# Kernel optimization log

Measured on AMD Instinct MI355X. Metric: run time of the kernel, lower is better.

Reference implementation:

```python
import jax, jax.numpy as jnp
import numpy as np

D_MODEL = 256; D_FFN = 1024; N_LEVELS = 4; N_HEADS = 8; N_POINTS = 4; N_VT = 8
D_HEAD = D_MODEL // N_HEADS
SHAPES = [(64, 64), (32, 32), (16, 16), (8, 8)]
L_SP = sum(h * w for h, w in SHAPES)  # 5440
BATCH = 4
EPS = 1e-5


def _ln(x, g, b):
    m = jnp.mean(x, -1, keepdims=True)
    xc = x - m
    v = jnp.mean(xc * xc, -1, keepdims=True)
    return g * xc * jax.lax.rsqrt(v + EPS) + b


def _bilinear(v_flat, x, y, H, W):
    # v_flat: (N, H*W, M, Dh); x, y: (N, Q, M) pixel coords (align_corners=False, zero padding)
    x0 = jnp.floor(x); y0 = jnp.floor(y)
    wx = x - x0; wy = y - y0
    out = 0.0
    for cx, cy, w in ((x0, y0, (1 - wx) * (1 - wy)), (x0 + 1, y0, wx * (1 - wy)),
                      (x0, y0 + 1, (1 - wx) * wy), (x0 + 1, y0 + 1, wx * wy)):
        valid = (cx >= 0) & (cx < W) & (cy >= 0) & (cy < H)
        xi = jnp.clip(cx, 0, W - 1).astype(jnp.int32)
        yi = jnp.clip(cy, 0, H - 1).astype(jnp.int32)
        idx = (yi * W + xi)[..., None]  # (N, Q, M, 1)
        g = jnp.take_along_axis(v_flat, idx, axis=1)  # (N, Q, M, Dh)
        out = out + (w * valid)[..., None] * g
    return out


def _msdeform_attn(query, ref, value_in, shapes_np, pad_mask, Wv, bv, Wo, bo, Wa, ba, Wp, bp):
    N, Lq, D = query.shape
    M, Lv, P, Dh = N_HEADS, N_LEVELS, N_POINTS, D_HEAD
    value = value_in @ Wv.T + bv
    value = jnp.where(pad_mask[..., None], 0.0, value)
    value = value.reshape(N, Lq, M, Dh)
    off = (query @ Wo.T + bo).reshape(N, Lq, M, Lv, P, 2)
    attn = jax.nn.softmax((query @ Wa.T + ba).reshape(N, Lq, M, Lv * P), axis=-1)
    attn = attn.reshape(N, Lq, M, Lv, P)
    # offset normalizer is (W, H) per level
    normalizer = jnp.asarray([[w, h] for h, w in shapes_np], jnp.float32)
    loc = ref[:, :, None, :, None, :] + off / normalizer[None, None, None, :, None, :]
    out = 0.0
    start = 0
    for l, (H, W) in enumerate(shapes_np):
        v_l = value[:, start:start + H * W]  # (N, H*W, M, Dh)
        x = (loc[:, :, :, l, :, 0] * W - 0.5).transpose(0, 1, 3, 2).reshape(N, Lq * P, M)
        y = (loc[:, :, :, l, :, 1] * H - 0.5).transpose(0, 1, 3, 2).reshape(N, Lq * P, M)
        samp = _bilinear(v_l, x, y, H, W).reshape(N, Lq, P, M, Dh)
        out = out + jnp.einsum('nqpmd,nqmp->nqmd', samp, attn[:, :, :, l, :])
        start += H * W
    return out.reshape(N, Lq, D) @ Wp.T + bp


def setup_inputs() -> dict:
    key = jax.random.key(0)
    ks = jax.random.split(key, 16)
    N, D = BATCH, D_MODEL
    Lq = L_SP + N_VT
    s = D ** -0.5
    rn = lambda k, sh, sc=1.0: jax.random.normal(k, sh, dtype=jnp.float32) * sc
    starts = np.cumsum([0] + [h * w for h, w in SHAPES[:-1]])
    return {
        'src': rn(ks[0], (N, L_SP, D)),
        'pos': rn(ks[1], (N, L_SP, D), 0.1),
        'reference_points': jax.random.uniform(ks[2], (N, Lq, N_LEVELS, 2), dtype=jnp.float32),
        'spatial_shapes': jnp.asarray(SHAPES, jnp.int32),
        'level_start_index': jnp.asarray(starts, jnp.int32),
        'padding_mask': jnp.zeros((N, Lq), bool),
        'all_vt': rn(ks[3], (N, 75 * N_VT, D)),
        'sel_vt': rn(ks[4], (N, N_VT, D)),
        'W_value': rn(ks[5], (D, D), s), 'b_value': jnp.zeros((D,), jnp.float32),
        'W_off': rn(ks[6], (N_HEADS * N_LEVELS * N_POINTS * 2, D), s),
        'b_off': rn(ks[7], (N_HEADS * N_LEVELS * N_POINTS * 2,), 0.1),
        'W_attn': rn(ks[8], (N_HEADS * N_LEVELS * N_POINTS, D), s),
        'b_attn': jnp.zeros((N_HEADS * N_LEVELS * N_POINTS,), jnp.float32),
        'W_out': rn(ks[9], (D, D), s), 'b_out': jnp.zeros((D,), jnp.float32),
        'g1': jnp.ones((D,), jnp.float32), 'beta1': jnp.zeros((D,), jnp.float32),
        'W1': rn(ks[10], (D_FFN, D), s), 'bf1': jnp.zeros((D_FFN,), jnp.float32),
        'W2': rn(ks[11], (D, D_FFN), D_FFN ** -0.5), 'bf2': jnp.zeros((D,), jnp.float32),
        'g2': jnp.ones((D,), jnp.float32), 'beta2': jnp.zeros((D,), jnp.float32),
    }


def reference(src, pos, reference_points, spatial_shapes, level_start_index, padding_mask,
              all_vt, sel_vt, W_value, b_value, W_off, b_off, W_attn, b_attn, W_out, b_out,
              g1, beta1, W1, bf1, W2, bf2, g2, beta2):
    shapes_np = [tuple(int(v) for v in row) for row in np.asarray(spatial_shapes)]
    q = jnp.concatenate([src + pos, sel_vt], axis=1)      # (N, Lq, D)
    v_in = jnp.concatenate([src, sel_vt], axis=1)
    src2 = _msdeform_attn(q, reference_points, v_in, shapes_np, padding_mask,
                          W_value, b_value, W_off, b_off, W_attn, b_attn, W_out, b_out)
    x = _ln(v_in + src2, g1, beta1)
    h = jax.nn.relu(x @ W1.T + bf1) @ W2.T + bf2
    x = _ln(x + h, g2, beta2)
    return (x[:, :L_SP, :], all_vt, x[:, L_SP:, :])
```

## Files before the change

kernel.cpp:

```cpp
#include <hip/hip_runtime.h>
#include <math.h>

#define NB   4
#define LQ   5448
#define LSP  5440
#define NR   21792
#define DM   256

typedef unsigned short u16;
typedef __attribute__((ext_vector_type(8))) short short8;
typedef __attribute__((ext_vector_type(4))) float f32x4;
typedef __attribute__((ext_vector_type(4))) unsigned int uint4v;

__device__ __forceinline__ u16 f2bf(float f) {
  unsigned int u = __float_as_uint(f);
  u = (u + 0x7fff + ((u >> 16) & 1)) >> 16;
  return (u16)u;
}
__device__ __forceinline__ float bf2f(u16 u) {
  return __uint_as_float(((unsigned int)u) << 16);
}

__device__ __forceinline__ void gld_lds16(const u16* g, u16* l) {
  __builtin_amdgcn_global_load_lds(
      (const __attribute__((address_space(1))) void*)g,
      (__attribute__((address_space(3))) void*)l, 16, 0, 0);
}

#define OFF_R0 0ull
#define OFF_R1 44630016ull
#define OFF_R2 55787520ull
#define OFF_R3 66945024ull
#define OFF_WB 78102528ull
#define OFF_BI 79609856ull

#define WOF_V  0
#define WOF_OA 65536
#define WOF_P  163840
#define WOF_1  229376
#define WOF_2  491520
#define NWELEM 753664

#define OUT0 5570560ull
#define OUT1 614400ull

__global__ __launch_bounds__(256) void convw_k(
    const float* __restrict__ Wv, const float* __restrict__ Wo,
    const float* __restrict__ Wa, const float* __restrict__ Wp,
    const float* __restrict__ W1, const float* __restrict__ W2,
    const float* __restrict__ bo, const float* __restrict__ ba,
    u16* __restrict__ out, float* __restrict__ boa)
{
  const int gid = blockIdx.x * 256 + threadIdx.x;
  if (gid < 384) boa[gid] = (gid < 256) ? bo[gid] : ba[gid - 256];
  if (gid >= NWELEM) return;
  float v;
  if (gid < WOF_OA) {
    v = Wv[gid];
  } else if (gid < WOF_P) {
    const int o = gid - WOF_OA;
    v = (o < 65536) ? Wo[o] : Wa[o - 65536];
  } else if (gid < WOF_1) {
    v = Wp[gid - WOF_P];
  } else if (gid < WOF_2) {
    v = W1[gid - WOF_1];
  } else {
    v = W2[gid - WOF_2];
  }
  out[gid] = f2bf(v);
}

__global__ __launch_bounds__(256) void qv_build_k(
    const float* __restrict__ src, const float* __restrict__ pos,
    const float* __restrict__ sel,
    u16* __restrict__ qb, u16* __restrict__ vb)
{
  const int row = blockIdx.x * 4 + (threadIdx.x >> 6);
  const int t = threadIdx.x & 63;
  const int n = row / LQ;
  const int i = row - n * LQ;
  float4 v, p = make_float4(0.f, 0.f, 0.f, 0.f);
  if (i < LSP) {
    const size_t o = ((size_t)(n * LSP + i)) * DM + t * 4;
    v = *(const float4*)(src + o);
    p = *(const float4*)(pos + o);
  } else {
    v = *(const float4*)(sel + ((size_t)(n * 8 + (i - LSP))) * DM + t * 4);
  }
  ushort4 vq, vv;
  vv.x = f2bf(v.x); vv.y = f2bf(v.y); vv.z = f2bf(v.z); vv.w = f2bf(v.w);
  vq.x = f2bf(v.x + p.x); vq.y = f2bf(v.y + p.y);
  vq.z = f2bf(v.z + p.z); vq.w = f2bf(v.w + p.w);
  *(ushort4*)(vb + (size_t)row * DM + t * 4) = vv;
  *(ushort4*)(qb + (size_t)row * DM + t * 4) = vq;
}

__global__ __launch_bounds__(256) void gemm_oa_k(
    const u16* __restrict__ A, int lda,
    const u16* __restrict__ B, int ldb,
    const float* __restrict__ bias,
    float* __restrict__ C, int ldc, int M, int K)
{
  __shared__ u16 As[128 * 32];
  __shared__ u16 Bs[128 * 32];
  const int tid = threadIdx.x;
  const int m0 = blockIdx.y * 128;
  const int n0 = blockIdx.x * 128;
  const int w = tid >> 6, lane = tid & 63;
  const int wy = w >> 1, wx = w & 1;
  const int l15 = lane & 15, quad = lane >> 4;
  const int lrow = lane >> 2;
  const int ga8 = ((lane & 3) ^ ((lane >> 3) & 3)) * 8;
  const int swz = (quad ^ ((l15 >> 1) & 3)) * 8;

  f32x4 acc[4][4] = {};

  for (int k0 = 0; k0 < K; k0 += 32) {
    for (int s = w; s < 8; s += 4) {
      int gm = m0 + s * 16 + lrow;
      if (gm >= M) gm = M - 1;
      gld_lds16(A + (size_t)gm * lda + k0 + ga8, &As[s * 512]);
    }
    for (int s = w; s < 8; s += 4) {
      gld_lds16(B + (size_t)(n0 + s * 16 + lrow) * ldb + k0 + ga8, &Bs[s * 512]);
    }
    __syncthreads();
    short8 af[4], bfr[4];
#pragma unroll
    for (int r = 0; r < 4; ++r)
      af[r] = *(const short8*)&As[(wy * 64 + r * 16 + l15) * 32 + swz];
#pragma unroll
    for (int c = 0; c < 4; ++c)
      bfr[c] = *(const short8*)&Bs[(wx * 64 + c * 16 + l15) * 32 + swz];
#pragma unroll
    for (int r = 0; r < 4; ++r)
#pragma unroll
      for (int c = 0; c < 4; ++c)
        acc[r][c] = __builtin_amdgcn_mfma_f32_16x16x32_bf16(af[r], bfr[c], acc[r][c], 0, 0, 0);
    __syncthreads();
  }

#pragma unroll
  for (int c = 0; c < 4; ++c) {
    const int cc = n0 + wx * 64 + c * 16 + l15;
    const float bb = bias[cc];
#pragma unroll
    for (int r = 0; r < 4; ++r) {
      const int rbase = m0 + wy * 64 + r * 16 + quad * 4;
#pragma unroll
      for (int j = 0; j < 4; ++j) {
        const int gr = rbase + j;
        if (gr < M) C[(size_t)gr * ldc + cc] = acc[r][c][j] + bb;
      }
    }
  }
}

template <int EPI>
__global__ __launch_bounds__(256) void gemmT_k(
    const u16* __restrict__ A, int lda,
    const u16* __restrict__ B, int ldb,
    const float* __restrict__ bias, int K,
    u16* __restrict__ outb, int ldob,
    const float* __restrict__ src, const float* __restrict__ sel,
    const u16* __restrict__ xbf,
    const float* __restrict__ gvec, const float* __restrict__ bvec,
    float* __restrict__ outf)
{
  __shared__ u16 As[64 * 32];
  __shared__ u16 Bs[256 * 32];
  const int tid = threadIdx.x;
  const int m0 = blockIdx.y * 64;
  const int n0 = blockIdx.x * 256;
  const int w = tid >> 6, lane = tid & 63;
  const int l15 = lane & 15, quad = lane >> 4;
  const int lrow = lane >> 2;
  const int ga8 = ((lane & 3) ^ ((lane >> 3) & 3)) * 8;
  const int swz = (quad ^ ((l15 >> 1) & 3)) * 8;

  f32x4 acc[4][4] = {};

  for (int k0 = 0; k0 < K; k0 += 32) {
    {
      int gm = m0 + w * 16 + lrow;
      if (gm >= NR) gm = NR - 1;
      gld_lds16(A + (size_t)gm * lda + k0 + ga8, &As[w * 512]);
    }
#pragma unroll
    for (int t = 0; t < 4; ++t) {
      const int s = w * 4 + t;
      gld_lds16(B + (size_t)(n0 + s * 16 + lrow) * ldb + k0 + ga8, &Bs[s * 512]);
    }
    __syncthreads();
    short8 af[4], bfr[4];
#pragma unroll
    for (int r = 0; r < 4; ++r)
      af[r] = *(const short8*)&As[(r * 16 + l15) * 32 + swz];
#pragma unroll
    for (int c = 0; c < 4; ++c)
      bfr[c] = *(const short8*)&Bs[(w * 64 + c * 16 + l15) * 32 + swz];
#pragma unroll
    for (int r = 0; r < 4; ++r)
#pragma unroll
      for (int c = 0; c < 4; ++c)
        acc[r][c] = __builtin_amdgcn_mfma_f32_16x16x32_bf16(af[r], bfr[c], acc[r][c], 0, 0, 0);
    __syncthreads();
  }

  int col[4];
  float bb[4];
#pragma unroll
  for (int c = 0; c < 4; ++c) {
    col[c] = n0 + w * 64 + c * 16 + l15;
    bb[c] = bias[col[c]];
  }

  if (EPI <= 1) {
#pragma unroll
    for (int c = 0; c < 4; ++c) {
#pragma unroll
      for (int r = 0; r < 4; ++r) {
#pragma unroll
        for (int j = 0; j < 4; ++j) {
          const int row = m0 + r * 16 + quad * 4 + j;
          if (row < NR) {
            float v = acc[r][c][j] + bb[c];
            if (EPI == 1) v = fmaxf(v, 0.f);
            outb[(size_t)row * ldob + col[c]] = f2bf(v);
          }
        }
      }
    }
    return;
  }

  float sv[4][4], sq[4][4];
#pragma unroll
  for (int r = 0; r < 4; ++r) {
#pragma unroll
    for (int j = 0; j < 4; ++j) {
      const int row = m0 + r * 16 + quad * 4 + j;
      const int rc = (row < NR) ? row : NR - 1;
      if (EPI == 2) {
        const int n = rc / LQ;
        const int i = rc - n * LQ;
        const float* resb = (i < LSP)
            ? src + ((size_t)(n * LSP + i)) * DM
            : sel + ((size_t)(n * 8 + (i - LSP))) * DM;
#pragma unroll
        for (int c = 0; c < 4; ++c) acc[r][c][j] += bb[c] + resb[col[c]];
      } else {
#pragma unroll
        for (int c = 0; c < 4; ++c)
          acc[r][c][j] += bb[c] + bf2f(xbf[(size_t)rc * DM + col[c]]);
      }
      float s = 0.f, q = 0.f;
#pragma unroll
      for (int c = 0; c < 4; ++c) {
        const float v = acc[r][c][j];
        s += v; q += v * v;
      }
      sv[r][j] = s; sq[r][j] = q;
    }
  }
#pragma unroll
  for (int off = 1; off < 16; off <<= 1) {
#pragma unroll
    for (int r = 0; r < 4; ++r)
#pragma unroll
      for (int j = 0; j < 4; ++j) {
        sv[r][j] += __shfl_xor(sv[r][j], off, 64);
        sq[r][j] += __shfl_xor(sq[r][j], off, 64);
      }
  }
  float* red = (float*)As;
  if (l15 == 0) {
#pragma unroll
    for (int r = 0; r < 4; ++r)
#pragma unroll
      for (int j = 0; j < 4; ++j) {
        const int rl = r * 16 + quad * 4 + j;
        red[(rl * 4 + w) * 2 + 0] = sv[r][j];
        red[(rl * 4 + w) * 2 + 1] = sq[r][j];
      }
  }
  __syncthreads();

  float gg[4], b2[4];
#pragma unroll
  for (int c = 0; c < 4; ++c) { gg[c] = gvec[col[c]]; b2[c] = bvec[col[c]]; }

#pragma unroll
  for (int r = 0; r < 4; ++r) {
#pragma unroll
    for (int j = 0; j < 4; ++j) {
      const int row = m0 + r * 16 + quad * 4 + j;
      if (row >= NR) continue;
      const int rl = r * 16 + quad * 4 + j;
      float ms = 0.f, mq = 0.f;
#pragma unroll
      for (int ww = 0; ww < 4; ++ww) {
        ms += red[(rl * 4 + ww) * 2 + 0];
        mq += red[(rl * 4 + ww) * 2 + 1];
      }
      const float mean = ms * (1.f / 256.f);
      const float var = mq * (1.f / 256.f) - mean * mean;
      const float rin = rsqrtf(var + 1e-5f);
      if (EPI == 2) {
#pragma unroll
        for (int c = 0; c < 4; ++c) {
          const float v = gg[c] * (acc[r][c][j] - mean) * rin + b2[c];
          outb[(size_t)row * DM + col[c]] = f2bf(v);
        }
      } else {
        const int n = row / LQ;
        const int i = row - n * LQ;
        float* dst = (i < LSP)
            ? outf + (size_t)(n * LSP + i) * DM
            : outf + OUT0 + OUT1 + (size_t)(n * 8 + (i - LSP)) * DM;
#pragma unroll
        for (int c = 0; c < 4; ++c)
          dst[col[c]] = gg[c] * (acc[r][c][j] - mean) * rin + b2[c];
      }
    }
  }
}

__device__ __forceinline__ void acc8(float* a, const u16* p, float w) {
  const uint4v u = *(const uint4v*)p;
  a[0] += w * __uint_as_float((u.x & 0xffffu) << 16);
  a[1] += w * __uint_as_float(u.x & 0xffff0000u);
  a[2] += w * __uint_as_float((u.y & 0xffffu) << 16);
  a[3] += w * __uint_as_float(u.y & 0xffff0000u);
  a[4] += w * __uint_as_float((u.z & 0xffffu) << 16);
  a[5] += w * __uint_as_float(u.z & 0xffff0000u);
  a[6] += w * __uint_as_float((u.w & 0xffffu) << 16);
  a[7] += w * __uint_as_float(u.w & 0xffff0000u);
}

__global__ __launch_bounds__(256) void sample3_k(
    const u16* __restrict__ value, const float* __restrict__ oa,
    const float* __restrict__ ref, u16* __restrict__ samp)
{
  const int lb = blockIdx.x;
  const int xcd = lb & 7;
  const int idx = lb >> 3;
  const int batch = xcd >> 1;
  const int rg = idx * 2 + (xcd & 1);
  if (rg >= 681) return;
  const int lane = threadIdx.x & 63;
  const int li = threadIdx.x & 31;
  const int m = li >> 2, q4 = li & 3;
  const int row = batch * LQ + rg * 8 + (threadIdx.x >> 5);

  const float* oar = oa + (size_t)row * 384;
  const float* offm = oar + m * 32;

  const float4 lg = *(const float4*)(oar + 256 + m * 16 + q4 * 4);
  float mx = fmaxf(fmaxf(lg.x, lg.y), fmaxf(lg.z, lg.w));
  mx = fmaxf(mx, __shfl_xor(mx, 1, 64));
  mx = fmaxf(mx, __shfl_xor(mx, 2, 64));
  const float e0 = __expf(lg.x - mx), e1 = __expf(lg.y - mx),
              e2 = __expf(lg.z - mx), e3 = __expf(lg.w - mx);
  float s = e0 + e1 + e2 + e3;
  s += __shfl_xor(s, 1, 64);
  s += __shfl_xor(s, 2, 64);
  const float inv = 1.f / s;
  float wp[4] = {e0 * inv, e1 * inv, e2 * inv, e3 * inv};

  const float4 r01 = *(const float4*)(ref + (size_t)row * 8);
  const float4 r23 = *(const float4*)(ref + (size_t)row * 8 + 4);
  const float RX[4] = {r01.x, r01.z, r23.x, r23.z};
  const float RY[4] = {r01.y, r01.w, r23.y, r23.w};
  const int HW[4] = {64, 32, 16, 8};
  const int ST[4] = {0, 4096, 5120, 5376};

  float a[8] = {};
#pragma unroll
  for (int l = 0; l < 4; ++l) {
    const int W = HW[l], H = HW[l];
    const float rx = RX[l], ry = RY[l];
    const u16* vb = value + ((size_t)(batch * LQ + ST[l])) * DM + m * 32 + q4 * 8;
    const float4 oA = *(const float4*)(offm + l * 8);
    const float4 oB = *(const float4*)(offm + l * 8 + 4);
    const float ox[4] = {oA.x, oA.z, oB.x, oB.z};
    const float oy[4] = {oA.y, oA.w, oB.y, oB.w};
#pragma unroll
    for (int p = 0; p < 4; ++p) {
      const float aw = __shfl(wp[p], (lane & ~3) | l, 64);
      const float px = rx * (float)W + ox[p] - 0.5f;
      const float py = ry * (float)H + oy[p] - 0.5f;
      const float xf = floorf(px), yf = floorf(py);
      const float wx = px - xf, wy = py - yf;
      const int x0 = (int)xf, y0 = (int)yf;
      const int x1 = x0 + 1, y1 = y0 + 1;
      const bool vx0 = (x0 >= 0) & (x0 < W), vx1 = (x1 >= 0) & (x1 < W);
      const bool vy0 = (y0 >= 0) & (y0 < H), vy1 = (y1 >= 0) & (y1 < H);
      if (vy0 & vx0) acc8(a, vb + (size_t)(y0 * W + x0) * DM, aw * (1.f - wx) * (1.f - wy));
      if (vy0 & vx1) acc8(a, vb + (size_t)(y0 * W + x1) * DM, aw * wx * (1.f - wy));
      if (vy1 & vx0) acc8(a, vb + (size_t)(y1 * W + x0) * DM, aw * (1.f - wx) * wy);
      if (vy1 & vx1) acc8(a, vb + (size_t)(y1 * W + x1) * DM, aw * wx * wy);
    }
  }
  uint4v ov;
  ov.x = (unsigned int)f2bf(a[0]) | ((unsigned int)f2bf(a[1]) << 16);
  ov.y = (unsigned int)f2bf(a[2]) | ((unsigned int)f2bf(a[3]) << 16);
  ov.z = (unsigned int)f2bf(a[4]) | ((unsigned int)f2bf(a[5]) << 16);
  ov.w = (unsigned int)f2bf(a[6]) | ((unsigned int)f2bf(a[7]) << 16);
  *(uint4v*)(samp + (size_t)row * DM + m * 32 + q4 * 8) = ov;
}

extern "C" void kernel_launch(void* const* d_in, const int* in_sizes, int n_in,
                              void* d_out, int out_size, void* d_ws, size_t ws_size,
                              hipStream_t stream)
{
  const float* src = (const float*)d_in[0];
  const float* pos = (const float*)d_in[1];
  const float* ref = (const float*)d_in[2];
  const float* all_vt = (const float*)d_in[6];
  const float* sel = (const float*)d_in[7];
  const float* Wv = (const float*)d_in[8];
  const float* bv = (const float*)d_in[9];
  const float* Wo = (const float*)d_in[10];
  const float* bo = (const float*)d_in[11];
  const float* Wa = (const float*)d_in[12];
  const float* ba = (const float*)d_in[13];
  const float* Wp = (const float*)d_in[14];
  const float* bp = (const float*)d_in[15];
  const float* g1 = (const float*)d_in[16];
  const float* be1 = (const float*)d_in[17];
  const float* W1 = (const float*)d_in[18];
  const float* b1 = (const float*)d_in[19];
  const float* W2 = (const float*)d_in[20];
  const float* b2 = (const float*)d_in[21];
  const float* g2 = (const float*)d_in[22];
  const float* be2 = (const float*)d_in[23];

  char* ws = (char*)d_ws;
  float* oabuf = (float*)(ws + OFF_R0);
  u16* h_bf    = (u16*)(ws + OFF_R0);
  u16* vin_bf  = (u16*)(ws + OFF_R1);
  u16* samp_bf = (u16*)(ws + OFF_R1);
  u16* q_bf    = (u16*)(ws + OFF_R2);
  u16* x_bf    = (u16*)(ws + OFF_R2);
  u16* val_bf  = (u16*)(ws + OFF_R3);
  u16* WB      = (u16*)(ws + OFF_WB);
  float* boa   = (float*)(ws + OFF_BI);

  const dim3 b256(256);
  const int MT64 = (NR + 63) / 64;
  const int MT128 = (NR + 127) / 128;

  convw_k<<<dim3((NWELEM + 255) / 256), b256, 0, stream>>>(
      Wv, Wo, Wa, Wp, W1, W2, bo, ba, WB, boa);
  qv_build_k<<<dim3(NR / 4), b256, 0, stream>>>(src, pos, sel, q_bf, vin_bf);
  gemmT_k<0><<<dim3(1, MT64), b256, 0, stream>>>(
      vin_bf, 256, WB + WOF_V, 256, bv, 256,
      val_bf, 256, nullptr, nullptr, nullptr, nullptr, nullptr, nullptr);
  gemm_oa_k<<<dim3(3, MT128), b256, 0, stream>>>(
      q_bf, 256, WB + WOF_OA, 256, boa, oabuf, 384, NR, 256);
  sample3_k<<<dim3(8 * 341), b256, 0, stream>>>(val_bf, oabuf, ref, samp_bf);
  gemmT_k<2><<<dim3(1, MT64), b256, 0, stream>>>(
      samp_bf, 256, WB + WOF_P, 256, bp, 256,
      x_bf, 256, src, sel, nullptr, g1, be1, nullptr);
  gemmT_k<1><<<dim3(4, MT64), b256, 0, stream>>>(
      x_bf, 256, WB + WOF_1, 256, b1, 256,
      h_bf, 1024, nullptr, nullptr, nullptr, nullptr, nullptr, nullptr);
  gemmT_k<3><<<dim3(1, MT64), b256, 0, stream>>>(
      h_bf, 1024, WB + WOF_2, 1024, b2, 1024,
      nullptr, 0, nullptr, nullptr, x_bf, g2, be2, (float*)d_out);
  hipMemcpyAsync((float*)d_out + OUT0, all_vt, OUT1 * sizeof(float),
                 hipMemcpyDeviceToDevice, stream);
}
```

Baseline: 325.1 us.

## Fuse q/v bf16 build into GEMM A-loads and restructure GEMM K pipeline

Removes the separate qv_build kernel: the value and offset/attention GEMMs now read fp32 src/pos/sel directly, add pos and convert to bf16 while staging the whole 64x256 A tile into LDS. A new templated gemmP keeps the full K-chunk of A resident and streams B through register double buffering across eight 32-wide k-steps, replacing the global_load_lds path. The offset/attention GEMM moves to a 384-thread block covering all 384 output columns. This saves a full bf16 write and reread of q and v_in, but it uses more LDS per block (up to 80 KB) and re-reads the fp32 A rows in each GEMM, which may lower occupancy.

Measured after the change: 317.5 us. -2.4%, faster.

```diff
diff --git a/kernel.cpp b/kernel.cpp
--- a/kernel.cpp
+++ b/kernel.cpp
@@ -20,11 +20,13 @@
 __device__ __forceinline__ float bf2f(u16 u) {
   return __uint_as_float(((unsigned int)u) << 16);
 }
-
-__device__ __forceinline__ void gld_lds16(const u16* g, u16* l) {
-  __builtin_amdgcn_global_load_lds(
-      (const __attribute__((address_space(1))) void*)g,
-      (__attribute__((address_space(3))) void*)l, 16, 0, 0);
+__device__ __forceinline__ uint4v pack8(float4 a, float4 b) {
+  uint4v r;
+  r.x = (unsigned)f2bf(a.x) | ((unsigned)f2bf(a.y) << 16);
+  r.y = (unsigned)f2bf(a.z) | ((unsigned)f2bf(a.w) << 16);
+  r.z = (unsigned)f2bf(b.x) | ((unsigned)f2bf(b.y) << 16);
+  r.w = (unsigned)f2bf(b.z) | ((unsigned)f2bf(b.w) << 16);
+  return r;
 }
 
 #define OFF_R0 0ull
@@ -70,141 +72,143 @@
   out[gid] = f2bf(v);
 }
 
-__global__ __launch_bounds__(256) void qv_build_k(
+template <int AMODE, int EPI, int BN>
+__global__ __launch_bounds__(BN) void gemmP(
+    const u16* __restrict__ A, int lda,
     const float* __restrict__ src, const float* __restrict__ pos,
     const float* __restrict__ sel,
-    u16* __restrict__ qb, u16* __restrict__ vb)
-{
-  const int row = blockIdx.x * 4 + (threadIdx.x >> 6);
-  const int t = threadIdx.x & 63;
-  const int n = row / LQ;
-  const int i = row - n * LQ;
-  float4 v, p = make_float4(0.f, 0.f, 0.f, 0.f);
-  if (i < LSP) {
-    const size_t o = ((size_t)(n * LSP + i)) * DM + t * 4;
-    v = *(const float4*)(src + o);
-    p = *(const float4*)(pos + o);
-  } else {
-    v = *(const float4*)(sel + ((size_t)(n * 8 + (i - LSP))) * DM + t * 4);
-  }
-  ushort4 vq, vv;
-  vv.x = f2bf(v.x); vv.y = f2bf(v.y); vv.z = f2bf(v.z); vv.w = f2bf(v.w);
-  vq.x = f2bf(v.x + p.x); vq.y = f2bf(v.y + p.y);
-  vq.z = f2bf(v.z + p.z); vq.w = f2bf(v.w + p.w);
-  *(ushort4*)(vb + (size_t)row * DM + t * 4) = vv;
-  *(ushort4*)(qb + (size_t)row * DM + t * 4) = vq;
-}
-
-__global__ __launch_bounds__(256) void gemm_oa_k(
-    const u16* __restrict__ A, int lda,
-    const u16* __restrict__ B, int ldb,
-    const float* __restrict__ bias,
-    float* __restrict__ C, int ldc, int M, int K)
-{
-  __shared__ u16 As[128 * 32];
-  __shared__ u16 Bs[128 * 32];
-  const int tid = threadIdx.x;
-  const int m0 = blockIdx.y * 128;
-  const int n0 = blockIdx.x * 128;
-  const int w = tid >> 6, lane = tid & 63;
-  const int wy = w >> 1, wx = w & 1;
-  const int l15 = lane & 15, quad = lane >> 4;
-  const int lrow = lane >> 2;
-  const int ga8 = ((lane & 3) ^ ((lane >> 3) & 3)) * 8;
-  const int swz = (quad ^ ((l15 >> 1) & 3)) * 8;
-
-  f32x4 acc[4][4] = {};
-
-  for (int k0 = 0; k0 < K; k0 += 32) {
-    for (int s = w; s < 8; s += 4) {
-      int gm = m0 + s * 16 + lrow;
-      if (gm >= M) gm = M - 1;
-      gld_lds16(A + (size_t)gm * lda + k0 + ga8, &As[s * 512]);
-    }
-    for (int s = w; s < 8; s += 4) {
-      gld_lds16(B + (size_t)(n0 + s * 16 + lrow) * ldb + k0 + ga8, &Bs[s * 512]);
-    }
-    __syncthreads();
-    short8 af[4], bfr[4];
-#pragma unroll
-    for (int r = 0; r < 4; ++r)
-      af[r] = *(const short8*)&As[(wy * 64 + r * 16 + l15) * 32 + swz];
-#pragma unroll
-    for (int c = 0; c < 4; ++c)
-      bfr[c] = *(const short8*)&Bs[(wx * 64 + c * 16 + l15) * 32 + swz];
-#pragma unroll
-    for (int r = 0; r < 4; ++r)
-#pragma unroll
-      for (int c = 0; c < 4; ++c)
-        acc[r][c] = __builtin_amdgcn_mfma_f32_16x16x32_bf16(af[r], bfr[c], acc[r][c], 0, 0, 0);
-    __syncthreads();
-  }
-
-#pragma unroll
-  for (int c = 0; c < 4; ++c) {
-    const int cc = n0 + wx * 64 + c * 16 + l15;
-    const float bb = bias[cc];
-#pragma unroll
-    for (int r = 0; r < 4; ++r) {
-      const int rbase = m0 + wy * 64 + r * 16 + quad * 4;
-#pragma unroll
-      for (int j = 0; j < 4; ++j) {
-        const int gr = rbase + j;
-        if (gr < M) C[(size_t)gr * ldc + cc] = acc[r][c][j] + bb;
-      }
-    }
-  }
-}
-
-template <int EPI>
-__global__ __launch_bounds__(256) void gemmT_k(
-    const u16* __restrict__ A, int lda,
     const u16* __restrict__ B, int ldb,
     const float* __restrict__ bias, int K,
     u16* __restrict__ outb, int ldob,
-    const float* __restrict__ src, const float* __restrict__ sel,
     const u16* __restrict__ xbf,
     const float* __restrict__ gvec, const float* __restrict__ bvec,
-    float* __restrict__ outf)
+    float* __restrict__ outf, int ldof)
 {
-  __shared__ u16 As[64 * 32];
-  __shared__ u16 Bs[256 * 32];
+  constexpr int NW = BN / 64;
+  __shared__ u16 As[64 * 256];
+  __shared__ u16 Bs[NW * 4096];
   const int tid = threadIdx.x;
-  const int m0 = blockIdx.y * 64;
-  const int n0 = blockIdx.x * 256;
   const int w = tid >> 6, lane = tid & 63;
   const int l15 = lane & 15, quad = lane >> 4;
-  const int lrow = lane >> 2;
-  const int ga8 = ((lane & 3) ^ ((lane >> 3) & 3)) * 8;
+  const int m0 = blockIdx.y * 64;
+  const int n0 = blockIdx.x * BN;
   const int swz = (quad ^ ((l15 >> 1) & 3)) * 8;
 
+  const int rA = (tid & 255) >> 2;
+  const int pA = tid & 3;
+  const int cA = (pA ^ ((rA >> 1) & 3)) * 8;
+  const int ldsA = rA * 32 + pA * 8;
+  int gmA = m0 + rA; if (gmA >= NR) gmA = NR - 1;
+  const float* aV = nullptr; const float* aP = nullptr;
+  if (AMODE) {
+    const int n = gmA / LQ, i = gmA - n * LQ;
+    if (i < LSP) {
+      aV = src + ((size_t)(n * LSP + i)) * DM;
+      if (AMODE == 1) aP = pos + ((size_t)(n * LSP + i)) * DM;
+    } else {
+      aV = sel + ((size_t)(n * 8 + (i - LSP))) * DM;
+    }
+  }
+
+  int rB[4], cB[4], lB[4];
+#pragma unroll
+  for (int i = 0; i < 4; ++i) {
+    const int g = lane + i * 64;
+    rB[i] = g >> 2;
+    const int p = g & 3;
+    cB[i] = (p ^ ((rB[i] >> 1) & 3)) * 8;
+    lB[i] = w * 4096 + rB[i] * 32 + p * 8;
+  }
+  const u16* Brow = B + (size_t)(n0 + w * 64) * ldb;
+
   f32x4 acc[4][4] = {};
 
-  for (int k0 = 0; k0 < K; k0 += 32) {
-    {
-      int gm = m0 + w * 16 + lrow;
-      if (gm >= NR) gm = NR - 1;
-      gld_lds16(A + (size_t)gm * lda + k0 + ga8, &As[w * 512]);
-    }
-#pragma unroll
-    for (int t = 0; t < 4; ++t) {
-      const int s = w * 4 + t;
-      gld_lds16(B + (size_t)(n0 + s * 16 + lrow) * ldb + k0 + ga8, &Bs[s * 512]);
+  for (int kc = 0; kc < K; kc += 256) {
+    if (kc) __syncthreads();
+    if (tid < 256) {
+      if (AMODE == 0) {
+        const u16* ap = A + (size_t)gmA * lda + kc + cA;
+#pragma unroll
+        for (int i = 0; i < 8; i += 4) {
+          uint4v t0 = *(const uint4v*)(ap + (i + 0) * 32);
+          uint4v t1 = *(const uint4v*)(ap + (i + 1) * 32);
+          uint4v t2 = *(const uint4v*)(ap + (i + 2) * 32);
+          uint4v t3 = *(const uint4v*)(ap + (i + 3) * 32);
+          *(uint4v*)&As[(i + 0) * 2048 + ldsA] = t0;
+          *(uint4v*)&As[(i + 1) * 2048 + ldsA] = t1;
+          *(uint4v*)&As[(i + 2) * 2048 + ldsA] = t2;
+          *(uint4v*)&As[(i + 3) * 2048 + ldsA] = t3;
+        }
+      } else {
+#pragma unroll
+        for (int i = 0; i < 8; i += 2) {
+          float4 v0a = *(const float4*)(aV + (i + 0) * 32 + cA);
+          float4 v0b = *(const float4*)(aV + (i + 0) * 32 + cA + 4);
+          float4 v1a = *(const float4*)(aV + (i + 1) * 32 + cA);
+          float4 v1b = *(const float4*)(aV + (i + 1) * 32 + cA + 4);
+          if (AMODE == 1 && aP) {
+            const float4 p0a = *(const float4*)(aP + (i + 0) * 32 + cA);
+            const float4 p0b = *(const float4*)(aP + (i + 0) * 32 + cA + 4);
+            const float4 p1a = *(const float4*)(aP + (i + 1) * 32 + cA);
+            const float4 p1b = *(const float4*)(aP + (i + 1) * 32 + cA + 4);
+            v0a.x += p0a.x; v0a.y += p0a.y; v0a.z += p0a.z; v0a.w += p0a.w;
+            v0b.x += p0b.x; v0b.y += p0b.y; v0b.z += p0b.z; v0b.w += p0b.w;
+            v1a.x += p1a.x; v1a.y += p1a.y; v1a.z += p1a.z; v1a.w += p1a.w;
+            v1b.x += p1b.x; v1b.y += p1b.y; v1b.z += p1b.z; v1b.w += p1b.w;
+          }
+          *(uint4v*)&As[(i + 0) * 2048 + ldsA] = pack8(v0a, v0b);
+          *(uint4v*)&As[(i + 1) * 2048 + ldsA] = pack8(v1a, v1b);
+        }
+      }
     }
     __syncthreads();
-    short8 af[4], bfr[4];
-#pragma unroll
-    for (int r = 0; r < 4; ++r)
-      af[r] = *(const short8*)&As[(r * 16 + l15) * 32 + swz];
-#pragma unroll
-    for (int c = 0; c < 4; ++c)
-      bfr[c] = *(const short8*)&Bs[(w * 64 + c * 16 + l15) * 32 + swz];
-#pragma unroll
-    for (int r = 0; r < 4; ++r)
+
+    uint4v rb0[4], rb1[4];
+#pragma unroll
+    for (int i = 0; i < 4; ++i)
+      rb0[i] = *(const uint4v*)(Brow + (size_t)rB[i] * ldb + kc + cB[i]);
+#pragma unroll
+    for (int i = 0; i < 4; ++i)
+      rb1[i] = *(const uint4v*)(Brow + (size_t)rB[i] * ldb + kc + 32 + cB[i]);
+#pragma unroll
+    for (int i = 0; i < 4; ++i) *(uint4v*)&Bs[lB[i]] = rb0[i];
+
+#pragma unroll
+    for (int j = 0; j < 8; ++j) {
+      if (j < 6) {
+        if ((j & 1) == 0) {
+#pragma unroll
+          for (int i = 0; i < 4; ++i)
+            rb0[i] = *(const uint4v*)(Brow + (size_t)rB[i] * ldb + kc + (j + 2) * 32 + cB[i]);
+        } else {
+#pragma unroll
+          for (int i = 0; i < 4; ++i)
+            rb1[i] = *(const uint4v*)(Brow + (size_t)rB[i] * ldb + kc + (j + 2) * 32 + cB[i]);
+        }
+      }
+      short8 af[4], bfr[4];
+#pragma unroll
+      for (int r = 0; r < 4; ++r)
+        af[r] = *(const short8*)&As[j * 2048 + (r * 16 + l15) * 32 + swz];
 #pragma unroll
       for (int c = 0; c < 4; ++c)
-        acc[r][c] = __builtin_amdgcn_mfma_f32_16x16x32_bf16(af[r], bfr[c], acc[r][c], 0, 0, 0);
-    __syncthreads();
+        bfr[c] = *(const short8*)&Bs[w * 4096 + (j & 1) * 2048 + (c * 16 + l15) * 32 + swz];
+      if (j < 7) {
+        const int buf = ((j + 1) & 1) * 2048;
+        if ((j & 1) == 0) {
+#pragma unroll
+          for (int i = 0; i < 4; ++i) *(uint4v*)&Bs[lB[i] + buf] = rb1[i];
+        } else {
+#pragma unroll
+          for (int i = 0; i < 4; ++i) *(uint4v*)&Bs[lB[i] + buf] = rb0[i];
+        }
+      }
+#pragma unroll
+      for (int r = 0; r < 4; ++r)
+#pragma unroll
+        for (int c = 0; c < 4; ++c)
+          acc[r][c] = __builtin_amdgcn_mfma_f32_16x16x32_bf16(af[r], bfr[c], acc[r][c], 0, 0, 0);
+    }
   }
 
   int col[4];
@@ -215,11 +219,24 @@
     bb[c] = bias[col[c]];
   }
 
+  if (EPI == 4) {
+#pragma unroll
+    for (int c = 0; c < 4; ++c)
+#pragma unroll
+      for (int r = 0; r < 4; ++r)
+#pragma unroll
+        for (int j = 0; j < 4; ++j) {
+          const int row = m0 + r * 16 + quad * 4 + j;
+          if (row < NR) outf[(size_t)row * ldof + col[c]] = acc[r][c][j] + bb[c];
+        }
+    return;
+  }
+
   if (EPI <= 1) {
 #pragma unroll
-    for (int c = 0; c < 4; ++c) {
-#pragma unroll
-      for (int r = 0; r < 4; ++r) {
+    for (int c = 0; c < 4; ++c)
+#pragma unroll
+      for (int r = 0; r < 4; ++r)
 #pragma unroll
         for (int j = 0; j < 4; ++j) {
           const int row = m0 + r * 16 + quad * 4 + j;
@@ -229,11 +246,10 @@
             outb[(size_t)row * ldob + col[c]] = f2bf(v);
           }
         }
-      }
-    }
     return;
   }
 
+  __syncthreads();
   float sv[4][4], sq[4][4];
 #pragma unroll
   for (int r = 0; r < 4; ++r) {
@@ -308,10 +324,9 @@
       const float rin = rsqrtf(var + 1e-5f);
       if (EPI == 2) {
 #pragma unroll
-        for (int c = 0; c < 4; ++c) {
-          const float v = gg[c] * (acc[r][c][j] - mean) * rin + b2[c];
-          outb[(size_t)row * DM + col[c]] = f2bf(v);
-        }
+        for (int c = 0; c < 4; ++c)
+          outb[(size_t)row * DM + col[c]] =
+              f2bf(gg[c] * (acc[r][c][j] - mean) * rin + b2[c]);
       } else {
         const int n = row / LQ;
         const int i = row - n * LQ;
@@ -439,36 +454,33 @@
   char* ws = (char*)d_ws;
   float* oabuf = (float*)(ws + OFF_R0);
   u16* h_bf    = (u16*)(ws + OFF_R0);
-  u16* vin_bf  = (u16*)(ws + OFF_R1);
   u16* samp_bf = (u16*)(ws + OFF_R1);
-  u16* q_bf    = (u16*)(ws + OFF_R2);
   u16* x_bf    = (u16*)(ws + OFF_R2);
   u16* val_bf  = (u16*)(ws + OFF_R3);
   u16* WB      = (u16*)(ws + OFF_WB);
   float* boa   = (float*)(ws + OFF_BI);
 
-  const dim3 b256(256);
+  const dim3 b256(256), b384(384);
   const int MT64 = (NR + 63) / 64;
-  const int MT128 = (NR + 127) / 128;
-
-  convw_k<<<dim3((NWELEM + 255) / 256), b256, 0, stream>>>(
+
+  convw_k<<<dim3(NWELEM / 256), b256, 0, stream>>>(
       Wv, Wo, Wa, Wp, W1, W2, bo, ba, WB, boa);
-  qv_build_k<<<dim3(NR / 4), b256, 0, stream>>>(src, pos, sel, q_bf, vin_bf);
-  gemmT_k<0><<<dim3(1, MT64), b256, 0, stream>>>(
-      vin_bf, 256, WB + WOF_V, 256, bv, 256,
-      val_bf, 256, nullptr, nullptr, nullptr, nullptr, nullptr, nullptr);
-  gemm_oa_k<<<dim3(3, MT128), b256, 0, stream>>>(
-      q_bf, 256, WB + WOF_OA, 256, boa, oabuf, 384, NR, 256);
+  gemmP<2, 0, 256><<<dim3(1, MT64), b256, 0, stream>>>(
+      nullptr, 0, src, nullptr, sel, WB + WOF_V, 256, bv, 256,
+      val_bf, 256, nullptr, nullptr, nullptr, nullptr, 0);
+  gemmP<1, 4, 384><<<dim3(1, MT64), b384, 0, stream>>>(
+      nullptr, 0, src, pos, sel, WB + WOF_OA, 256, boa, 256,
+      nullptr, 0, nullptr, nullptr, nullptr, oabuf, 384);
   sample3_k<<<dim3(8 * 341), b256, 0, stream>>>(val_bf, oabuf, ref, samp_bf);
-  gemmT_k<2><<<dim3(1, MT64), b256, 0, stream>>>(
-      samp_bf, 256, WB + WOF_P, 256, bp, 256,
-      x_bf, 256, src, sel, nullptr, g1, be1, nullptr);
-  gemmT_k<1><<<dim3(4, MT64), b256, 0, stream>>>(
-      x_bf, 256, WB + WOF_1, 256, b1, 256,
-      h_bf, 1024, nullptr, nullptr, nullptr, nullptr, nullptr, nullptr);
-  gemmT_k<3><<<dim3(1, MT64), b256, 0, stream>>>(
-      h_bf, 1024, WB + WOF_2, 1024, b2, 1024,
-      nullptr, 0, nullptr, nullptr, x_bf, g2, be2, (float*)d_out);
+  gemmP<0, 2, 256><<<dim3(1, MT64), b256, 0, stream>>>(
+      samp_bf, 256, src, nullptr, sel, WB + WOF_P, 256, bp, 256,
+      x_bf, 256, nullptr, g1, be1, nullptr, 0);
+  gemmP<0, 1, 256><<<dim3(4, MT64), b256, 0, stream>>>(
+      x_bf, 256, nullptr, nullptr, nullptr, WB + WOF_1, 256, b1, 256,
+      h_bf, 1024, nullptr, nullptr, nullptr, nullptr, 0);
+  gemmP<0, 3, 256><<<dim3(1, MT64), b256, 0, stream>>>(
+      h_bf, 1024, nullptr, nullptr, nullptr, WB + WOF_2, 1024, b2, 1024,
+      nullptr, 0, x_bf, g2, be2, (float*)d_out, 0);
   hipMemcpyAsync((float*)d_out + OUT0, all_vt, OUT1 * sizeof(float),
                  hipMemcpyDeviceToDevice, stream);
 }
```
